# Kernel optimization log

Measured on AMD Instinct MI355X. Metric: run time of the kernel, lower is better.

Reference implementation:

```python
import jax, jax.numpy as jnp
import numpy as np

B, S, D, H, E = 1, 2048, 1024, 16, 65536
HD = D // H
LN_EPS = 1e-5


def setup_inputs() -> dict:
    key = jax.random.key(0)
    ks = jax.random.split(key, 18)
    s = 0.02
    inp = {
        'x': jax.random.normal(ks[0], (B, S, D), jnp.float32),
        'node_types': jax.random.uniform(ks[1], (B, S, 2), jnp.float32),
        'stoichiometry': jax.random.normal(ks[2], (E,), jnp.float32),
        'Wq': s * jax.random.normal(ks[3], (D, D), jnp.float32),
        'bq': jnp.zeros((D,), jnp.float32),
        'Wk': s * jax.random.normal(ks[4], (D, D), jnp.float32),
        'bk': jnp.zeros((D,), jnp.float32),
        'Wv': s * jax.random.normal(ks[5], (D, D), jnp.float32),
        'bv': jnp.zeros((D,), jnp.float32),
        'Wo': s * jax.random.normal(ks[6], (D, D), jnp.float32),
        'bo': jnp.zeros((D,), jnp.float32),
        'Wn1': s * jax.random.normal(ks[7], (D // 2, D + 2), jnp.float32),
        'bn1': jnp.zeros((D // 2,), jnp.float32),
        'Wn2': s * jax.random.normal(ks[8], (H, D // 2), jnp.float32),
        'bn2': jnp.zeros((H,), jnp.float32),
        'ln_g': jnp.ones((D,), jnp.float32),
        'ln_b': jnp.zeros((D,), jnp.float32),
        'edge_index': jax.random.randint(ks[9], (2, E), 0, S, jnp.int64),
    }
    return inp


def _layer_norm(y, g, b):
    m = jnp.mean(y, axis=-1, keepdims=True)
    v = jnp.mean(jnp.square(y - m), axis=-1, keepdims=True)
    return (y - m) * jax.lax.rsqrt(v + LN_EPS) * g + b


def reference(x, node_types, stoichiometry, Wq, bq, Wk, bk, Wv, bv, Wo, bo,
              Wn1, bn1, Wn2, bn2, ln_g, ln_b, edge_index):
    b, s, d = x.shape
    h, hd = H, d // H
    # QKV projections -> [b, h, s, hd]
    Q = (x @ Wq.T + bq).reshape(b, s, h, hd).transpose(0, 2, 1, 3)
    K = (x @ Wk.T + bk).reshape(b, s, h, hd).transpose(0, 2, 1, 3)
    V = (x @ Wv.T + bv).reshape(b, s, h, hd).transpose(0, 2, 1, 3)
    scores = jnp.einsum('bhqd,bhkd->bhqk', Q, K) / np.sqrt(hd)  # [b,h,s,s]
    # node-type attention MLP -> per-node, per-head weights [b,s,h]
    nt_in = jnp.concatenate([x, node_types], axis=-1)
    ntw = jax.nn.softmax(jax.nn.relu(nt_in @ Wn1.T + bn1) @ Wn2.T + bn2, axis=-1)
    # applied as per-head, per-key multiplicative mask [b,h,1,s]
    scores = scores * ntw.transpose(0, 2, 1)[:, :, None, :]
    # dense stoichiometric mask via edge scatter [s,s]
    stoich_mask = jnp.zeros((s, s), x.dtype).at[edge_index[0], edge_index[1]].set(stoichiometry)
    scores = scores * stoich_mask[None, None]
    attn = jax.nn.softmax(scores, axis=-1)  # dropout = identity (eval)
    out = jnp.einsum('bhqk,bhkd->bhqd', attn, V).transpose(0, 2, 1, 3).reshape(b, s, d)
    out = out @ Wo.T + bo
    y = _layer_norm(x + out, ln_g, ln_b)
    return (y, attn)
```

## Files before the change

### kernel.cpp

```cpp
#include <hip/hip_runtime.h>
#include <hip/hip_bf16.h>

#define S 2048
#define D 1024
#define NH 16
#define HD 64
#define NE 65536
#define DH 512
#define SLOTS 128

typedef __attribute__((ext_vector_type(8))) short short8;
typedef __attribute__((ext_vector_type(4))) float f32x4;

#define MFMA16(a, b, c) __builtin_amdgcn_mfma_f32_16x16x32_bf16(a, b, c, 0, 0, 0)

__device__ __forceinline__ unsigned short f2bf(float f) {
    __hip_bfloat16 h = __float2bfloat16(f);
    return *reinterpret_cast<unsigned short*>(&h);
}
__device__ __forceinline__ float bf2f(unsigned short u) {
    unsigned int x = ((unsigned int)u) << 16;
    return *reinterpret_cast<float*>(&x);
}

__device__ __forceinline__ void gload16(const unsigned short* g, unsigned short* l) {
    __builtin_amdgcn_global_load_lds(
        (const __attribute__((address_space(1))) unsigned int*)g,
        (__attribute__((address_space(3))) unsigned int*)l, 16, 0, 0);
}

__global__ __launch_bounds__(256) void k_prep(const float* __restrict__ x,
                                              const float* __restrict__ Wq,
                                              const float* __restrict__ Wk,
                                              const float* __restrict__ Wv,
                                              const float* __restrict__ Wn1,
                                              const float* __restrict__ Wo,
                                              const float* __restrict__ bq,
                                              const float* __restrict__ bk,
                                              const float* __restrict__ bv,
                                              const float* __restrict__ bn1,
                                              unsigned short* __restrict__ xb,
                                              unsigned short* __restrict__ wb,
                                              float* __restrict__ biasAll,
                                              int* __restrict__ rowcnt,
                                              float* __restrict__ vsumf) {
    int row = blockIdx.x, z = blockIdx.y, t = threadIdx.x;
    if (z == 5) {
        if (row < 14) {
            int g = row * 256 + t;
            float v = (g < 1024) ? bq[g]
                    : (g < 2048) ? bk[g - 1024]
                    : (g < 3072) ? bv[g - 2048] : bn1[g - 3072];
            biasAll[g] = v;
        } else if (row >= 16 && row < 24) {
            rowcnt[(row - 16) * 256 + t] = 0;
        } else if (row >= 24 && row < 28) {
            vsumf[(row - 24) * 256 + t] = 0.f;
        }
        return;
    }
    if (z >= 6) {
        int s = (z - 6) * 1024 + row;
        const float* r = x + (long)s * 1024;
        unsigned short* o = xb + (long)s * 1024;
#pragma unroll
        for (int j = 0; j < 4; j++) o[t * 4 + j] = f2bf(r[t * 4 + j]);
        return;
    }
    if (z == 3 && row >= DH) return;
    const float* src;
    long stride = 1024;
    if (z == 0) src = Wq;
    else if (z == 1) src = Wk;
    else if (z == 2) src = Wv;
    else if (z == 3) { src = Wn1; stride = 1026; }
    else src = Wo;
    const float* r = src + (long)row * stride;
    unsigned short* o = wb + (long)z * 1048576 + (long)row * 1024;
#pragma unroll
    for (int j = 0; j < 4; j++) o[t * 4 + j] = f2bf(r[t * 4 + j]);
}

__global__ __launch_bounds__(256) void k_gemm_fused(const unsigned short* __restrict__ A,
                                                    const unsigned short* __restrict__ Bw,
                                                    const float* __restrict__ biasAll,
                                                    const int* __restrict__ ei,
                                                    const float* __restrict__ st,
                                                    int* __restrict__ rowcnt,
                                                    int* __restrict__ cpack,
                                                    float* __restrict__ cval,
                                                    float* __restrict__ vsumf,
                                                    unsigned short* __restrict__ qout,
                                                    unsigned short* __restrict__ kout,
                                                    unsigned short* __restrict__ vout,
                                                    float* __restrict__ hidden) {
    if (blockIdx.y == 28) {
        int base = blockIdx.x * 4096 + threadIdx.x;
#pragma unroll
        for (int k = 0; k < 16; k++) {
            int e = base + k * 256;
            int r = ei[e], c = ei[NE + e];
            int i = atomicAdd(&rowcnt[r], 1);
            if (i < SLOTS) {
                cpack[r * SLOTS + i] = ((e + 1) << 11) | c;
                cval[r * SLOTS + i] = st[e];
            }
        }
        return;
    }
    __shared__ unsigned short Als[128 * 64];
    __shared__ unsigned short Bls[128 * 64];
    const int tid = threadIdx.x, w = tid >> 6, lane = tid & 63;
    const int l15 = lane & 15, lhi = lane >> 4;
    const int wr = w >> 1, wc = w & 1;
    const int m0 = blockIdx.x * 128, n0 = blockIdx.y * 128;
    f32x4 acc[4][4] = {};
    for (int kt = 0; kt < 16; kt++) {
        __syncthreads();
#pragma unroll
        for (int i = 0; i < 4; i++) {
            int reg = i * 4 + w;
            int idx = reg * 64 + lane;
            int row = idx >> 3, c8 = (idx & 7) * 8;
            gload16(A + (long)(m0 + row) * 1024 + kt * 64 + c8, Als + reg * 512);
            gload16(Bw + (long)(n0 + row) * 1024 + kt * 64 + c8, Bls + reg * 512);
        }
        asm volatile("s_waitcnt vmcnt(0)");
        __syncthreads();
#pragma unroll
        for (int kk = 0; kk < 2; kk++) {
            short8 a[4], b[4];
#pragma unroll
            for (int mi = 0; mi < 4; mi++)
                a[mi] = *reinterpret_cast<const short8*>(Als + (wr * 64 + mi * 16 + l15) * 64 + kk * 32 + lhi * 8);
#pragma unroll
            for (int ni = 0; ni < 4; ni++)
                b[ni] = *reinterpret_cast<const short8*>(Bls + (wc * 64 + ni * 16 + l15) * 64 + kk * 32 + lhi * 8);
#pragma unroll
            for (int mi = 0; mi < 4; mi++)
#pragma unroll
                for (int ni = 0; ni < 4; ni++)
                    acc[mi][ni] = MFMA16(a[mi], b[ni], acc[mi][ni]);
        }
    }
#pragma unroll
    for (int ni = 0; ni < 4; ni++) {
        int n = n0 + wc * 64 + ni * 16 + l15;
        float bb = biasAll[n];
        float colsum = 0.f;
#pragma unroll
        for (int mi = 0; mi < 4; mi++) {
#pragma unroll
            for (int r = 0; r < 4; r++) {
                int m = m0 + wr * 64 + mi * 16 + lhi * 4 + r;
                float v = acc[mi][ni][r] + bb;
                colsum += v;
                if (n < 3072) {
                    int z = n >> 10, c = n & 1023;
                    int hh = c >> 6, hd = c & 63;
                    unsigned short* dst = (z == 0) ? qout : ((z == 1) ? kout : vout);
                    dst[(long)hh * S * HD + (long)m * HD + hd] = f2bf(v);
                } else {
                    hidden[(long)m * DH + (n - 3072)] = v;
                }
            }
        }
        if (n >= 2048 && n < 3072) {
            colsum += __shfl_xor(colsum, 16);
            colsum += __shfl_xor(colsum, 32);
            if (lhi == 0) atomicAdd(&vsumf[n - 2048], colsum);
        }
    }
}

__global__ __launch_bounds__(256) void k_gemm_out(const unsigned short* __restrict__ A,
                                                  const unsigned short* __restrict__ Bw,
                                                  const float* __restrict__ bo,
                                                  float* __restrict__ proj) {
    __shared__ unsigned short Als[128 * 64];
    __shared__ unsigned short Bls[64 * 64];
    const int tid = threadIdx.x, w = tid >> 6, lane = tid & 63;
    const int l15 = lane & 15, lhi = lane >> 4;
    const int wr = w >> 1, wc = w & 1;
    const int m0 = blockIdx.x * 128, n0 = blockIdx.y * 64;
    f32x4 acc[4][2] = {};
    for (int kt = 0; kt < 16; kt++) {
        __syncthreads();
#pragma unroll
        for (int i = 0; i < 4; i++) {
            int reg = i * 4 + w;
            int idx = reg * 64 + lane;
            int row = idx >> 3, c8 = (idx & 7) * 8;
            gload16(A + (long)(m0 + row) * 1024 + kt * 64 + c8, Als + reg * 512);
        }
#pragma unroll
        for (int i = 0; i < 2; i++) {
            int reg = i * 4 + w;
            int idx = reg * 64 + lane;
            int row = idx >> 3, c8 = (idx & 7) * 8;
            gload16(Bw + (long)(n0 + row) * 1024 + kt * 64 + c8, Bls + reg * 512);
        }
        asm volatile("s_waitcnt vmcnt(0)");
        __syncthreads();
#pragma unroll
        for (int kk = 0; kk < 2; kk++) {
            short8 a[4], b[2];
#pragma unroll
            for (int mi = 0; mi < 4; mi++)
                a[mi] = *reinterpret_cast<const short8*>(Als + (wr * 64 + mi * 16 + l15) * 64 + kk * 32 + lhi * 8);
#pragma unroll
            for (int ni = 0; ni < 2; ni++)
                b[ni] = *reinterpret_cast<const short8*>(Bls + (wc * 32 + ni * 16 + l15) * 64 + kk * 32 + lhi * 8);
#pragma unroll
            for (int mi = 0; mi < 4; mi++)
#pragma unroll
                for (int ni = 0; ni < 2; ni++)
                    acc[mi][ni] = MFMA16(a[mi], b[ni], acc[mi][ni]);
        }
    }
#pragma unroll
    for (int ni = 0; ni < 2; ni++) {
        int n = n0 + wc * 32 + ni * 16 + l15;
        float bb = bo[n];
#pragma unroll
        for (int mi = 0; mi < 4; mi++) {
#pragma unroll
            for (int r = 0; r < 4; r++) {
                int m = m0 + wr * 64 + mi * 16 + lhi * 4 + r;
                proj[(long)m * 1024 + n] = acc[mi][ni][r] + bb;
            }
        }
    }
}

__global__ __launch_bounds__(256) void k_ntw(const float* __restrict__ hidden,
                                             const float* __restrict__ Wn1,
                                             const float* __restrict__ nt,
                                             const float* __restrict__ Wn2,
                                             const float* __restrict__ bn2,
                                             float* __restrict__ ntwT) {
    int tid = threadIdx.x;
    int s = blockIdx.x;
    __shared__ float rh[DH];
    __shared__ float part[16][17];
    float nt0 = nt[s * 2 + 0], nt1 = nt[s * 2 + 1];
    for (int j = tid; j < DH; j += 256) {
        float v = hidden[(long)s * DH + j] + nt0 * Wn1[(long)j * 1026 + 1024]
                + nt1 * Wn1[(long)j * 1026 + 1025];
        rh[j] = fmaxf(v, 0.f);
    }
    __syncthreads();
    {
        int hh = tid & 15, ch = tid >> 4;
        float p2 = 0.f;
#pragma unroll
        for (int j = 0; j < 32; j++) p2 += rh[ch * 32 + j] * Wn2[hh * DH + ch * 32 + j];
        part[ch][hh] = p2;
    }
    __syncthreads();
    if (tid < 16) {
        float l = bn2[tid];
#pragma unroll
        for (int c = 0; c < 16; c++) l += part[c][tid];
        float mx = l;
#pragma unroll
        for (int m = 1; m < 16; m <<= 1) mx = fmaxf(mx, __shfl_xor(mx, m));
        float e = __expf(l - mx);
        float sum = e;
#pragma unroll
        for (int m = 1; m < 16; m <<= 1) sum += __shfl_xor(sum, m);
        ntwT[tid * S + s] = e / sum;
    }
}

__global__ __launch_bounds__(256, 4) void k_sparsefill(const unsigned short* __restrict__ qb,
                                                       const unsigned short* __restrict__ kb,
                                                       const unsigned short* __restrict__ vb,
                                                       const float* __restrict__ ntwT,
                                                       const int* __restrict__ rowcnt,
                                                       const int* __restrict__ cpack,
                                                       const float* __restrict__ cval,
                                                       const float* __restrict__ vsumf,
                                                       float* __restrict__ attn_out,
                                                       unsigned short* __restrict__ pv_out) {
    __shared__ int c_lds[4][SLOTS];
    __shared__ float pd_lds[4][SLOTS];
    __shared__ unsigned char alive_lds[4][SLOTS];
    const int tid = threadIdx.x, w = tid >> 6, lane = tid & 63;
    int b = (int)blockIdx.x;
    b = (b & 7) * 1024 + (b >> 3);
    const int r = b * 4 + w;
    const int h = r >> 11, q = r & 2047;
    const int i_loc = lane & 15, dpart = lane >> 4;
    const int nnz_raw = rowcnt[q];
    const int nnz = nnz_raw < SLOTS ? nnz_raw : SLOTS;
    const int chunks = (nnz + 15) >> 4;

    for (int i = lane; i < nnz; i += 64) c_lds[w][i] = cpack[q * SLOTS + i];
    asm volatile("" ::: "memory");

    int myCnt = 0;
    for (int i = lane; i < nnz; i += 64) {
        int pk = c_lds[w][i];
        bool alive = true;
        for (int j = 0; j < nnz; j++) {
            int pj = c_lds[w][j];
            if ((((pj ^ pk) & 2047) == 0) && pj > pk) alive = false;
        }
        alive_lds[w][i] = alive ? 1 : 0;
        myCnt += alive ? 1 : 0;
    }
#pragma unroll
    for (int off = 1; off < 64; off <<= 1) myCnt += __shfl_xor(myCnt, off);
    const int nnz_alive = myCnt;
    asm volatile("" ::: "memory");

    float qf[16];
    {
        const unsigned short* qp = qb + ((long)h * S + q) * HD + dpart * 16;
        short8 q0 = *reinterpret_cast<const short8*>(qp);
        short8 q1 = *reinterpret_cast<const short8*>(qp + 8);
#pragma unroll
        for (int j = 0; j < 8; j++) {
            qf[j] = bf2f((unsigned short)q0[j]);
            qf[8 + j] = bf2f((unsigned short)q1[j]);
        }
    }

    float s_reg[8], e_reg[8];
    int c_reg[8];
    int vmask = 0;
#pragma unroll
    for (int c8 = 0; c8 < 8; c8++) {
        s_reg[c8] = -3.0e38f;
        c_reg[c8] = 0;
        if (c8 < chunks) {
            int i = c8 * 16 + i_loc;
            bool inr = i < nnz;
            int ig = inr ? i : 0;
            bool valid = inr && alive_lds[w][ig];
            int c = c_lds[w][ig] & 2047;
            float vv = cval[q * SLOTS + ig];
            const unsigned short* kp = kb + ((long)h * S + c) * HD + dpart * 16;
            short8 k0 = *reinterpret_cast<const short8*>(kp);
            short8 k1 = *reinterpret_cast<const short8*>(kp + 8);
            float dot = 0.f;
#pragma unroll
            for (int j = 0; j < 8; j++) {
                dot += qf[j] * bf2f((unsigned short)k0[j]);
                dot += qf[8 + j] * bf2f((unsigned short)k1[j]);
            }
            dot += __shfl_xor(dot, 16);
            dot += __shfl_xor(dot, 32);
            if (valid) {
                s_reg[c8] = dot * 0.125f * ntwT[(long)h * S + c] * vv;
                c_reg[c8] = c;
                vmask |= 1 << c8;
            }
        }
    }

    float m = s_reg[0];
#pragma unroll
    for (int c8 = 1; c8 < 8; c8++) m = fmaxf(m, s_reg[c8]);
    m = fmaxf(m, __shfl_xor(m, 1));
    m = fmaxf(m, __shfl_xor(m, 2));
    m = fmaxf(m, __shfl_xor(m, 4));
    m = fmaxf(m, __shfl_xor(m, 8));
    const float gm = fmaxf(m, 0.f);

    float zs = 0.f;
#pragma unroll
    for (int c8 = 0; c8 < 8; c8++) {
        e_reg[c8] = __expf(s_reg[c8] - gm);
        zs += e_reg[c8];
    }
    zs += __shfl_xor(zs, 1);
    zs += __shfl_xor(zs, 2);
    zs += __shfl_xor(zs, 4);
    zs += __shfl_xor(zs, 8);
    const float e0 = __expf(-gm);
    const float Z = zs + (float)(S - nnz_alive) * e0;
    const float inv = 1.0f / Z;
    const float p0 = e0 * inv;

    if (dpart == 0) {
#pragma unroll
        for (int c8 = 0; c8 < 8; c8++) {
            int i = c8 * 16 + i_loc;
            if (c8 < chunks && i < nnz)
                pd_lds[w][i] = ((vmask >> c8) & 1) ? e_reg[c8] * inv - p0 : 0.f;
        }
    }
    asm volatile("" ::: "memory");

    float* arow = attn_out + (long)r * S;
    f32x4* a4 = reinterpret_cast<f32x4*>(arow) + lane;
    const f32x4 f4 = {p0, p0, p0, p0};
#pragma unroll
    for (int u = 0; u < 8; u++) __builtin_nontemporal_store(f4, a4 + u * 64);
    __threadfence_block();
    if (dpart == 0) {
#pragma unroll
        for (int c8 = 0; c8 < 8; c8++)
            if ((vmask >> c8) & 1) arow[c_reg[c8]] = e_reg[c8] * inv;
    }

    float vacc = 0.f;
    for (int i = 0; i < nnz; i++) {
        int c = c_lds[w][i] & 2047;
        float pd = pd_lds[w][i];
        vacc += pd * bf2f(vb[((long)h * S + c) * HD + lane]);
    }
    vacc += p0 * vsumf[h * HD + lane];
    pv_out[(long)q * D + h * HD + lane] = f2bf(vacc);
}

__global__ __launch_bounds__(256) void k_ln(const float* __restrict__ x,
                                            const float* __restrict__ proj,
                                            const float* __restrict__ g,
                                            const float* __restrict__ bta,
                                            float* __restrict__ y) {
    int s = blockIdx.x, tid = threadIdx.x;
    int w = tid >> 6, lane = tid & 63;
    __shared__ float red[8];
    float4 xv = reinterpret_cast<const float4*>(x + (long)s * 1024)[tid];
    float4 pv = reinterpret_cast<const float4*>(proj + (long)s * 1024)[tid];
    float t0 = xv.x + pv.x, t1 = xv.y + pv.y, t2 = xv.z + pv.z, t3 = xv.w + pv.w;
    float lsum = t0 + t1 + t2 + t3;
#pragma unroll
    for (int m = 32; m >= 1; m >>= 1) lsum += __shfl_xor(lsum, m);
    if (lane == 0) red[w] = lsum;
    __syncthreads();
    float mean = (red[0] + red[1] + red[2] + red[3]) * (1.0f / 1024.f);
    float d0 = t0 - mean, d1 = t1 - mean, d2 = t2 - mean, d3 = t3 - mean;
    float lvar = d0 * d0 + d1 * d1 + d2 * d2 + d3 * d3;
#pragma unroll
    for (int m = 32; m >= 1; m >>= 1) lvar += __shfl_xor(lvar, m);
    if (lane == 0) red[4 + w] = lvar;
    __syncthreads();
    float var = (red[4] + red[5] + red[6] + red[7]) * (1.0f / 1024.f);
    float rstd = rsqrtf(var + 1e-5f);
    float4 gv = reinterpret_cast<const float4*>(g)[tid];
    float4 bv = reinterpret_cast<const float4*>(bta)[tid];
    float4 out;
    out.x = d0 * rstd * gv.x + bv.x;
    out.y = d1 * rstd * gv.y + bv.y;
    out.z = d2 * rstd * gv.z + bv.z;
    out.w = d3 * rstd * gv.w + bv.w;
    reinterpret_cast<float4*>(y + (long)s * 1024)[tid] = out;
}

extern "C" void kernel_launch(void* const* d_in, const int* in_sizes, int n_in,
                              void* d_out, int out_size, void* d_ws, size_t ws_size,
                              hipStream_t stream) {
    const float* x = (const float*)d_in[0];
    const float* node_types = (const float*)d_in[1];
    const float* stoich = (const float*)d_in[2];
    const float* Wq = (const float*)d_in[3];
    const float* bq = (const float*)d_in[4];
    const float* Wk = (const float*)d_in[5];
    const float* bk = (const float*)d_in[6];
    const float* Wv = (const float*)d_in[7];
    const float* bv = (const float*)d_in[8];
    const float* Wo = (const float*)d_in[9];
    const float* bo = (const float*)d_in[10];
    const float* Wn1 = (const float*)d_in[11];
    const float* bn1 = (const float*)d_in[12];
    const float* Wn2 = (const float*)d_in[13];
    const float* bn2 = (const float*)d_in[14];
    const float* ln_g = (const float*)d_in[15];
    const float* ln_b = (const float*)d_in[16];
    const int* ei = (const int*)d_in[17];

    char* ws = (char*)d_ws;
    unsigned short* x_bf = (unsigned short*)(ws);
    unsigned short* q_bf = (unsigned short*)(ws + (4l << 20));
    unsigned short* k_bf = (unsigned short*)(ws + (8l << 20));
    unsigned short* v_bf = (unsigned short*)(ws + (12l << 20));
    unsigned short* w_bf = (unsigned short*)(ws + (16l << 20));
    float* hidden = (float*)(ws + (26l << 20));
    float* ntwT = (float*)(ws + (30l << 20));
    int* rowcnt = (int*)(ws + (30l << 20) + (192l << 10));
    float* vsumf = (float*)(ws + (30l << 20) + (384l << 10));
    float* biasAll = (float*)(ws + (30l << 20) + (448l << 10));
    int* cpack = (int*)(ws + (31l << 20));
    float* cval = (float*)(ws + (32l << 20));
    unsigned short* pvb = (unsigned short*)(ws + (49l << 20));
    float* proj = (float*)(ws + (53l << 20));

    float* y_out = (float*)d_out;
    float* attn_out = (float*)d_out + (long)S * D;

    k_prep<<<dim3(1024, 8), 256, 0, stream>>>(x, Wq, Wk, Wv, Wn1, Wo,
                                              bq, bk, bv, bn1, x_bf, w_bf,
                                              biasAll, rowcnt, vsumf);
    k_gemm_fused<<<dim3(16, 29), 256, 0, stream>>>(x_bf, w_bf, biasAll,
                                                   ei, stoich, rowcnt, cpack, cval,
                                                   vsumf, q_bf, k_bf, v_bf, hidden);
    k_ntw<<<2048, 256, 0, stream>>>(hidden, Wn1, node_types, Wn2, bn2, ntwT);
    k_sparsefill<<<8192, 256, 0, stream>>>(q_bf, k_bf, v_bf, ntwT, rowcnt,
                                           cpack, cval, vsumf, attn_out, pvb);
    k_gemm_out<<<dim3(16, 16), 256, 0, stream>>>(pvb, w_bf + 4l * 1048576, bo, proj);
    k_ln<<<2048, 256, 0, stream>>>(x, proj, ln_g, ln_b, y_out);
}
```

Before: 154.9 us.

## Fuse all stages into one cooperative persistent kernel with grid syncs

Replaces the six separate kernel launches (prep, fused QKV GEMM plus edge bucketing, ntw MLP, sparse fill, output GEMM, layernorm) with a single cooperative kernel. Stages are separated by grid.sync and work items are distributed over a persistent grid of up to 512 blocks. The aim is to remove per-launch overhead and inter-kernel gaps. In exchange, occupancy is capped at two blocks per CU, blocks loop over work items, and every grid-wide barrier costs time and can expose load imbalance.

After: 498.9 us. 222% more time.

```diff
diff --git a/kernel.cpp b/kernel.cpp
--- a/kernel.cpp
+++ b/kernel.cpp
@@ -1,5 +1,8 @@
 #include <hip/hip_runtime.h>
+#include <hip/hip_cooperative_groups.h>
 #include <hip/hip_bf16.h>
+
+namespace cg = cooperative_groups;
 
 #define S 2048
 #define D 1024
@@ -29,478 +32,457 @@
         (__attribute__((address_space(3))) unsigned int*)l, 16, 0, 0);
 }
 
-__global__ __launch_bounds__(256) void k_prep(const float* __restrict__ x,
-                                              const float* __restrict__ Wq,
-                                              const float* __restrict__ Wk,
-                                              const float* __restrict__ Wv,
-                                              const float* __restrict__ Wn1,
-                                              const float* __restrict__ Wo,
-                                              const float* __restrict__ bq,
-                                              const float* __restrict__ bk,
-                                              const float* __restrict__ bv,
-                                              const float* __restrict__ bn1,
-                                              unsigned short* __restrict__ xb,
-                                              unsigned short* __restrict__ wb,
-                                              float* __restrict__ biasAll,
-                                              int* __restrict__ rowcnt,
-                                              float* __restrict__ vsumf) {
-    int row = blockIdx.x, z = blockIdx.y, t = threadIdx.x;
-    if (z == 5) {
-        if (row < 14) {
-            int g = row * 256 + t;
-            float v = (g < 1024) ? bq[g]
-                    : (g < 2048) ? bk[g - 1024]
-                    : (g < 3072) ? bv[g - 2048] : bn1[g - 3072];
-            biasAll[g] = v;
-        } else if (row >= 16 && row < 24) {
-            rowcnt[(row - 16) * 256 + t] = 0;
-        } else if (row >= 24 && row < 28) {
-            vsumf[(row - 24) * 256 + t] = 0.f;
-        }
-        return;
-    }
-    if (z >= 6) {
-        int s = (z - 6) * 1024 + row;
-        const float* r = x + (long)s * 1024;
-        unsigned short* o = xb + (long)s * 1024;
-#pragma unroll
-        for (int j = 0; j < 4; j++) o[t * 4 + j] = f2bf(r[t * 4 + j]);
-        return;
-    }
-    if (z == 3 && row >= DH) return;
-    const float* src;
-    long stride = 1024;
-    if (z == 0) src = Wq;
-    else if (z == 1) src = Wk;
-    else if (z == 2) src = Wv;
-    else if (z == 3) { src = Wn1; stride = 1026; }
-    else src = Wo;
-    const float* r = src + (long)row * stride;
-    unsigned short* o = wb + (long)z * 1048576 + (long)row * 1024;
-#pragma unroll
-    for (int j = 0; j < 4; j++) o[t * 4 + j] = f2bf(r[t * 4 + j]);
-}
-
-__global__ __launch_bounds__(256) void k_gemm_fused(const unsigned short* __restrict__ A,
-                                                    const unsigned short* __restrict__ Bw,
-                                                    const float* __restrict__ biasAll,
-                                                    const int* __restrict__ ei,
-                                                    const float* __restrict__ st,
-                                                    int* __restrict__ rowcnt,
-                                                    int* __restrict__ cpack,
-                                                    float* __restrict__ cval,
-                                                    float* __restrict__ vsumf,
-                                                    unsigned short* __restrict__ qout,
-                                                    unsigned short* __restrict__ kout,
-                                                    unsigned short* __restrict__ vout,
-                                                    float* __restrict__ hidden) {
-    if (blockIdx.y == 28) {
-        int base = blockIdx.x * 4096 + threadIdx.x;
-#pragma unroll
-        for (int k = 0; k < 16; k++) {
-            int e = base + k * 256;
-            int r = ei[e], c = ei[NE + e];
-            int i = atomicAdd(&rowcnt[r], 1);
-            if (i < SLOTS) {
-                cpack[r * SLOTS + i] = ((e + 1) << 11) | c;
-                cval[r * SLOTS + i] = st[e];
-            }
-        }
-        return;
-    }
-    __shared__ unsigned short Als[128 * 64];
-    __shared__ unsigned short Bls[128 * 64];
-    const int tid = threadIdx.x, w = tid >> 6, lane = tid & 63;
+struct Params {
+    const float *x, *nt, *st;
+    const float *Wq, *bq, *Wk, *bk, *Wv, *bv, *Wo, *bo;
+    const float *Wn1, *bn1, *Wn2, *bn2, *ln_g, *ln_b;
+    const int* ei;
+    unsigned short *xb, *wb, *qb, *kb, *vb, *pvb;
+    float *hidden, *ntwT, *vsumf, *biasAll, *cval, *proj, *attn, *y;
+    int *rowcnt, *cpack;
+};
+
+__global__ __launch_bounds__(256, 2) void k_mega(Params p) {
+    __shared__ __align__(16) unsigned char smem[32768];
+    cg::grid_group grid = cg::this_grid();
+    const int tid = threadIdx.x;
+    const int nb = gridDim.x, bid = blockIdx.x;
+    const int w = tid >> 6, lane = tid & 63;
     const int l15 = lane & 15, lhi = lane >> 4;
-    const int wr = w >> 1, wc = w & 1;
-    const int m0 = blockIdx.x * 128, n0 = blockIdx.y * 128;
-    f32x4 acc[4][4] = {};
-    for (int kt = 0; kt < 16; kt++) {
-        __syncthreads();
-#pragma unroll
-        for (int i = 0; i < 4; i++) {
-            int reg = i * 4 + w;
-            int idx = reg * 64 + lane;
-            int row = idx >> 3, c8 = (idx & 7) * 8;
-            gload16(A + (long)(m0 + row) * 1024 + kt * 64 + c8, Als + reg * 512);
-            gload16(Bw + (long)(n0 + row) * 1024 + kt * 64 + c8, Bls + reg * 512);
-        }
-        asm volatile("s_waitcnt vmcnt(0)");
-        __syncthreads();
-#pragma unroll
-        for (int kk = 0; kk < 2; kk++) {
-            short8 a[4], b[4];
-#pragma unroll
-            for (int mi = 0; mi < 4; mi++)
-                a[mi] = *reinterpret_cast<const short8*>(Als + (wr * 64 + mi * 16 + l15) * 64 + kk * 32 + lhi * 8);
-#pragma unroll
-            for (int ni = 0; ni < 4; ni++)
-                b[ni] = *reinterpret_cast<const short8*>(Bls + (wc * 64 + ni * 16 + l15) * 64 + kk * 32 + lhi * 8);
-#pragma unroll
-            for (int mi = 0; mi < 4; mi++)
-#pragma unroll
-                for (int ni = 0; ni < 4; ni++)
-                    acc[mi][ni] = MFMA16(a[mi], b[ni], acc[mi][ni]);
-        }
-    }
-#pragma unroll
-    for (int ni = 0; ni < 4; ni++) {
-        int n = n0 + wc * 64 + ni * 16 + l15;
-        float bb = biasAll[n];
-        float colsum = 0.f;
-#pragma unroll
-        for (int mi = 0; mi < 4; mi++) {
-#pragma unroll
-            for (int r = 0; r < 4; r++) {
-                int m = m0 + wr * 64 + mi * 16 + lhi * 4 + r;
-                float v = acc[mi][ni][r] + bb;
-                colsum += v;
-                if (n < 3072) {
-                    int z = n >> 10, c = n & 1023;
-                    int hh = c >> 6, hd = c & 63;
-                    unsigned short* dst = (z == 0) ? qout : ((z == 1) ? kout : vout);
-                    dst[(long)hh * S * HD + (long)m * HD + hd] = f2bf(v);
-                } else {
-                    hidden[(long)m * DH + (n - 3072)] = v;
-                }
-            }
-        }
-        if (n >= 2048 && n < 3072) {
-            colsum += __shfl_xor(colsum, 16);
-            colsum += __shfl_xor(colsum, 32);
-            if (lhi == 0) atomicAdd(&vsumf[n - 2048], colsum);
-        }
-    }
-}
-
-__global__ __launch_bounds__(256) void k_gemm_out(const unsigned short* __restrict__ A,
-                                                  const unsigned short* __restrict__ Bw,
-                                                  const float* __restrict__ bo,
-                                                  float* __restrict__ proj) {
-    __shared__ unsigned short Als[128 * 64];
-    __shared__ unsigned short Bls[64 * 64];
-    const int tid = threadIdx.x, w = tid >> 6, lane = tid & 63;
-    const int l15 = lane & 15, lhi = lane >> 4;
-    const int wr = w >> 1, wc = w & 1;
-    const int m0 = blockIdx.x * 128, n0 = blockIdx.y * 64;
-    f32x4 acc[4][2] = {};
-    for (int kt = 0; kt < 16; kt++) {
-        __syncthreads();
-#pragma unroll
-        for (int i = 0; i < 4; i++) {
-            int reg = i * 4 + w;
-            int idx = reg * 64 + lane;
-            int row = idx >> 3, c8 = (idx & 7) * 8;
-            gload16(A + (long)(m0 + row) * 1024 + kt * 64 + c8, Als + reg * 512);
-        }
-#pragma unroll
-        for (int i = 0; i < 2; i++) {
-            int reg = i * 4 + w;
-            int idx = reg * 64 + lane;
-            int row = idx >> 3, c8 = (idx & 7) * 8;
-            gload16(Bw + (long)(n0 + row) * 1024 + kt * 64 + c8, Bls + reg * 512);
-        }
-        asm volatile("s_waitcnt vmcnt(0)");
-        __syncthreads();
-#pragma unroll
-        for (int kk = 0; kk < 2; kk++) {
-            short8 a[4], b[2];
-#pragma unroll
-            for (int mi = 0; mi < 4; mi++)
-                a[mi] = *reinterpret_cast<const short8*>(Als + (wr * 64 + mi * 16 + l15) * 64 + kk * 32 + lhi * 8);
-#pragma unroll
-            for (int ni = 0; ni < 2; ni++)
-                b[ni] = *reinterpret_cast<const short8*>(Bls + (wc * 32 + ni * 16 + l15) * 64 + kk * 32 + lhi * 8);
-#pragma unroll
-            for (int mi = 0; mi < 4; mi++)
-#pragma unroll
-                for (int ni = 0; ni < 2; ni++)
-                    acc[mi][ni] = MFMA16(a[mi], b[ni], acc[mi][ni]);
-        }
-    }
-#pragma unroll
-    for (int ni = 0; ni < 2; ni++) {
-        int n = n0 + wc * 32 + ni * 16 + l15;
-        float bb = bo[n];
-#pragma unroll
-        for (int mi = 0; mi < 4; mi++) {
-#pragma unroll
-            for (int r = 0; r < 4; r++) {
-                int m = m0 + wr * 64 + mi * 16 + lhi * 4 + r;
-                proj[(long)m * 1024 + n] = acc[mi][ni][r] + bb;
-            }
-        }
-    }
-}
-
-__global__ __launch_bounds__(256) void k_ntw(const float* __restrict__ hidden,
-                                             const float* __restrict__ Wn1,
-                                             const float* __restrict__ nt,
-                                             const float* __restrict__ Wn2,
-                                             const float* __restrict__ bn2,
-                                             float* __restrict__ ntwT) {
-    int tid = threadIdx.x;
-    int s = blockIdx.x;
-    __shared__ float rh[DH];
-    __shared__ float part[16][17];
-    float nt0 = nt[s * 2 + 0], nt1 = nt[s * 2 + 1];
-    for (int j = tid; j < DH; j += 256) {
-        float v = hidden[(long)s * DH + j] + nt0 * Wn1[(long)j * 1026 + 1024]
-                + nt1 * Wn1[(long)j * 1026 + 1025];
-        rh[j] = fmaxf(v, 0.f);
-    }
-    __syncthreads();
+
+    for (int u = bid; u < 8192; u += nb) {
+        int row = u & 1023, z = u >> 10;
+        if (z == 5) {
+            if (row < 14) {
+                int g = row * 256 + tid;
+                float v = (g < 1024) ? p.bq[g]
+                        : (g < 2048) ? p.bk[g - 1024]
+                        : (g < 3072) ? p.bv[g - 2048] : p.bn1[g - 3072];
+                p.biasAll[g] = v;
+            } else if (row >= 16 && row < 24) {
+                p.rowcnt[(row - 16) * 256 + tid] = 0;
+            } else if (row >= 24 && row < 28) {
+                p.vsumf[(row - 24) * 256 + tid] = 0.f;
+            }
+            continue;
+        }
+        if (z >= 6) {
+            int s = (z - 6) * 1024 + row;
+            const float* r = p.x + (long)s * 1024;
+            unsigned short* o = p.xb + (long)s * 1024;
+#pragma unroll
+            for (int j = 0; j < 4; j++) o[tid * 4 + j] = f2bf(r[tid * 4 + j]);
+            continue;
+        }
+        if (z == 3 && row >= DH) continue;
+        const float* src;
+        long stride = 1024;
+        if (z == 0) src = p.Wq;
+        else if (z == 1) src = p.Wk;
+        else if (z == 2) src = p.Wv;
+        else if (z == 3) { src = p.Wn1; stride = 1026; }
+        else src = p.Wo;
+        const float* r = src + (long)row * stride;
+        unsigned short* o = p.wb + (long)z * 1048576 + (long)row * 1024;
+#pragma unroll
+        for (int j = 0; j < 4; j++) o[tid * 4 + j] = f2bf(r[tid * 4 + j]);
+    }
+    grid.sync();
+
     {
-        int hh = tid & 15, ch = tid >> 4;
-        float p2 = 0.f;
-#pragma unroll
-        for (int j = 0; j < 32; j++) p2 += rh[ch * 32 + j] * Wn2[hh * DH + ch * 32 + j];
-        part[ch][hh] = p2;
-    }
-    __syncthreads();
-    if (tid < 16) {
-        float l = bn2[tid];
-#pragma unroll
-        for (int c = 0; c < 16; c++) l += part[c][tid];
-        float mx = l;
-#pragma unroll
-        for (int m = 1; m < 16; m <<= 1) mx = fmaxf(mx, __shfl_xor(mx, m));
-        float e = __expf(l - mx);
-        float sum = e;
-#pragma unroll
-        for (int m = 1; m < 16; m <<= 1) sum += __shfl_xor(sum, m);
-        ntwT[tid * S + s] = e / sum;
-    }
-}
-
-__global__ __launch_bounds__(256, 4) void k_sparsefill(const unsigned short* __restrict__ qb,
-                                                       const unsigned short* __restrict__ kb,
-                                                       const unsigned short* __restrict__ vb,
-                                                       const float* __restrict__ ntwT,
-                                                       const int* __restrict__ rowcnt,
-                                                       const int* __restrict__ cpack,
-                                                       const float* __restrict__ cval,
-                                                       const float* __restrict__ vsumf,
-                                                       float* __restrict__ attn_out,
-                                                       unsigned short* __restrict__ pv_out) {
-    __shared__ int c_lds[4][SLOTS];
-    __shared__ float pd_lds[4][SLOTS];
-    __shared__ unsigned char alive_lds[4][SLOTS];
-    const int tid = threadIdx.x, w = tid >> 6, lane = tid & 63;
-    int b = (int)blockIdx.x;
-    b = (b & 7) * 1024 + (b >> 3);
-    const int r = b * 4 + w;
-    const int h = r >> 11, q = r & 2047;
-    const int i_loc = lane & 15, dpart = lane >> 4;
-    const int nnz_raw = rowcnt[q];
-    const int nnz = nnz_raw < SLOTS ? nnz_raw : SLOTS;
-    const int chunks = (nnz + 15) >> 4;
-
-    for (int i = lane; i < nnz; i += 64) c_lds[w][i] = cpack[q * SLOTS + i];
-    asm volatile("" ::: "memory");
-
-    int myCnt = 0;
-    for (int i = lane; i < nnz; i += 64) {
-        int pk = c_lds[w][i];
-        bool alive = true;
-        for (int j = 0; j < nnz; j++) {
-            int pj = c_lds[w][j];
-            if ((((pj ^ pk) & 2047) == 0) && pj > pk) alive = false;
-        }
-        alive_lds[w][i] = alive ? 1 : 0;
-        myCnt += alive ? 1 : 0;
-    }
-#pragma unroll
-    for (int off = 1; off < 64; off <<= 1) myCnt += __shfl_xor(myCnt, off);
-    const int nnz_alive = myCnt;
-    asm volatile("" ::: "memory");
-
-    float qf[16];
+        unsigned short* Als = (unsigned short*)smem;
+        unsigned short* Bls = (unsigned short*)(smem + 16384);
+        const int wr = w >> 1, wc = w & 1;
+        for (int u = bid; u < 464; u += nb) {
+            if (u >= 448) {
+                int base = (u - 448) * 4096 + tid;
+#pragma unroll
+                for (int k = 0; k < 16; k++) {
+                    int e = base + k * 256;
+                    int r = p.ei[e], c = p.ei[NE + e];
+                    int i = atomicAdd(&p.rowcnt[r], 1);
+                    if (i < SLOTS) {
+                        p.cpack[r * SLOTS + i] = ((e + 1) << 11) | c;
+                        p.cval[r * SLOTS + i] = p.st[e];
+                    }
+                }
+                continue;
+            }
+            const int m0 = (u & 15) * 128, n0 = (u >> 4) * 128;
+            f32x4 acc[4][4] = {};
+            for (int kt = 0; kt < 16; kt++) {
+                __syncthreads();
+#pragma unroll
+                for (int i = 0; i < 4; i++) {
+                    int reg = i * 4 + w;
+                    int idx = reg * 64 + lane;
+                    int row = idx >> 3, c8 = (idx & 7) * 8;
+                    gload16(p.xb + (long)(m0 + row) * 1024 + kt * 64 + c8, Als + reg * 512);
+                    gload16(p.wb + (long)(n0 + row) * 1024 + kt * 64 + c8, Bls + reg * 512);
+                }
+                asm volatile("s_waitcnt vmcnt(0)");
+                __syncthreads();
+#pragma unroll
+                for (int kk = 0; kk < 2; kk++) {
+                    short8 a[4], b[4];
+#pragma unroll
+                    for (int mi = 0; mi < 4; mi++)
+                        a[mi] = *reinterpret_cast<const short8*>(Als + (wr * 64 + mi * 16 + l15) * 64 + kk * 32 + lhi * 8);
+#pragma unroll
+                    for (int ni = 0; ni < 4; ni++)
+                        b[ni] = *reinterpret_cast<const short8*>(Bls + (wc * 64 + ni * 16 + l15) * 64 + kk * 32 + lhi * 8);
+#pragma unroll
+                    for (int mi = 0; mi < 4; mi++)
+#pragma unroll
+                        for (int ni = 0; ni < 4; ni++)
+                            acc[mi][ni] = MFMA16(a[mi], b[ni], acc[mi][ni]);
+                }
+            }
+#pragma unroll
+            for (int ni = 0; ni < 4; ni++) {
+                int n = n0 + wc * 64 + ni * 16 + l15;
+                float bb = p.biasAll[n];
+                float colsum = 0.f;
+#pragma unroll
+                for (int mi = 0; mi < 4; mi++) {
+#pragma unroll
+                    for (int r = 0; r < 4; r++) {
+                        int m = m0 + wr * 64 + mi * 16 + lhi * 4 + r;
+                        float v = acc[mi][ni][r] + bb;
+                        colsum += v;
+                        if (n < 3072) {
+                            int z = n >> 10, c = n & 1023;
+                            int hh = c >> 6, hd = c & 63;
+                            unsigned short* dst = (z == 0) ? p.qb : ((z == 1) ? p.kb : p.vb);
+                            dst[(long)hh * S * HD + (long)m * HD + hd] = f2bf(v);
+                        } else {
+                            p.hidden[(long)m * DH + (n - 3072)] = v;
+                        }
+                    }
+                }
+                if (n >= 2048 && n < 3072) {
+                    colsum += __shfl_xor(colsum, 16);
+                    colsum += __shfl_xor(colsum, 32);
+                    if (lhi == 0) atomicAdd(&p.vsumf[n - 2048], colsum);
+                }
+            }
+        }
+    }
+    grid.sync();
+
     {
-        const unsigned short* qp = qb + ((long)h * S + q) * HD + dpart * 16;
-        short8 q0 = *reinterpret_cast<const short8*>(qp);
-        short8 q1 = *reinterpret_cast<const short8*>(qp + 8);
-#pragma unroll
-        for (int j = 0; j < 8; j++) {
-            qf[j] = bf2f((unsigned short)q0[j]);
-            qf[8 + j] = bf2f((unsigned short)q1[j]);
-        }
-    }
-
-    float s_reg[8], e_reg[8];
-    int c_reg[8];
-    int vmask = 0;
-#pragma unroll
-    for (int c8 = 0; c8 < 8; c8++) {
-        s_reg[c8] = -3.0e38f;
-        c_reg[c8] = 0;
-        if (c8 < chunks) {
-            int i = c8 * 16 + i_loc;
-            bool inr = i < nnz;
-            int ig = inr ? i : 0;
-            bool valid = inr && alive_lds[w][ig];
-            int c = c_lds[w][ig] & 2047;
-            float vv = cval[q * SLOTS + ig];
-            const unsigned short* kp = kb + ((long)h * S + c) * HD + dpart * 16;
-            short8 k0 = *reinterpret_cast<const short8*>(kp);
-            short8 k1 = *reinterpret_cast<const short8*>(kp + 8);
-            float dot = 0.f;
-#pragma unroll
-            for (int j = 0; j < 8; j++) {
-                dot += qf[j] * bf2f((unsigned short)k0[j]);
-                dot += qf[8 + j] * bf2f((unsigned short)k1[j]);
-            }
-            dot += __shfl_xor(dot, 16);
-            dot += __shfl_xor(dot, 32);
-            if (valid) {
-                s_reg[c8] = dot * 0.125f * ntwT[(long)h * S + c] * vv;
-                c_reg[c8] = c;
-                vmask |= 1 << c8;
-            }
-        }
-    }
-
-    float m = s_reg[0];
-#pragma unroll
-    for (int c8 = 1; c8 < 8; c8++) m = fmaxf(m, s_reg[c8]);
-    m = fmaxf(m, __shfl_xor(m, 1));
-    m = fmaxf(m, __shfl_xor(m, 2));
-    m = fmaxf(m, __shfl_xor(m, 4));
-    m = fmaxf(m, __shfl_xor(m, 8));
-    const float gm = fmaxf(m, 0.f);
-
-    float zs = 0.f;
-#pragma unroll
-    for (int c8 = 0; c8 < 8; c8++) {
-        e_reg[c8] = __expf(s_reg[c8] - gm);
-        zs += e_reg[c8];
-    }
-    zs += __shfl_xor(zs, 1);
-    zs += __shfl_xor(zs, 2);
-    zs += __shfl_xor(zs, 4);
-    zs += __shfl_xor(zs, 8);
-    const float e0 = __expf(-gm);
-    const float Z = zs + (float)(S - nnz_alive) * e0;
-    const float inv = 1.0f / Z;
-    const float p0 = e0 * inv;
-
-    if (dpart == 0) {
-#pragma unroll
-        for (int c8 = 0; c8 < 8; c8++) {
-            int i = c8 * 16 + i_loc;
-            if (c8 < chunks && i < nnz)
-                pd_lds[w][i] = ((vmask >> c8) & 1) ? e_reg[c8] * inv - p0 : 0.f;
-        }
-    }
-    asm volatile("" ::: "memory");
-
-    float* arow = attn_out + (long)r * S;
-    f32x4* a4 = reinterpret_cast<f32x4*>(arow) + lane;
-    const f32x4 f4 = {p0, p0, p0, p0};
-#pragma unroll
-    for (int u = 0; u < 8; u++) __builtin_nontemporal_store(f4, a4 + u * 64);
-    __threadfence_block();
-    if (dpart == 0) {
-#pragma unroll
-        for (int c8 = 0; c8 < 8; c8++)
-            if ((vmask >> c8) & 1) arow[c_reg[c8]] = e_reg[c8] * inv;
-    }
-
-    float vacc = 0.f;
-    for (int i = 0; i < nnz; i++) {
-        int c = c_lds[w][i] & 2047;
-        float pd = pd_lds[w][i];
-        vacc += pd * bf2f(vb[((long)h * S + c) * HD + lane]);
-    }
-    vacc += p0 * vsumf[h * HD + lane];
-    pv_out[(long)q * D + h * HD + lane] = f2bf(vacc);
-}
-
-__global__ __launch_bounds__(256) void k_ln(const float* __restrict__ x,
-                                            const float* __restrict__ proj,
-                                            const float* __restrict__ g,
-                                            const float* __restrict__ bta,
-                                            float* __restrict__ y) {
-    int s = blockIdx.x, tid = threadIdx.x;
-    int w = tid >> 6, lane = tid & 63;
-    __shared__ float red[8];
-    float4 xv = reinterpret_cast<const float4*>(x + (long)s * 1024)[tid];
-    float4 pv = reinterpret_cast<const float4*>(proj + (long)s * 1024)[tid];
-    float t0 = xv.x + pv.x, t1 = xv.y + pv.y, t2 = xv.z + pv.z, t3 = xv.w + pv.w;
-    float lsum = t0 + t1 + t2 + t3;
-#pragma unroll
-    for (int m = 32; m >= 1; m >>= 1) lsum += __shfl_xor(lsum, m);
-    if (lane == 0) red[w] = lsum;
-    __syncthreads();
-    float mean = (red[0] + red[1] + red[2] + red[3]) * (1.0f / 1024.f);
-    float d0 = t0 - mean, d1 = t1 - mean, d2 = t2 - mean, d3 = t3 - mean;
-    float lvar = d0 * d0 + d1 * d1 + d2 * d2 + d3 * d3;
-#pragma unroll
-    for (int m = 32; m >= 1; m >>= 1) lvar += __shfl_xor(lvar, m);
-    if (lane == 0) red[4 + w] = lvar;
-    __syncthreads();
-    float var = (red[4] + red[5] + red[6] + red[7]) * (1.0f / 1024.f);
-    float rstd = rsqrtf(var + 1e-5f);
-    float4 gv = reinterpret_cast<const float4*>(g)[tid];
-    float4 bv = reinterpret_cast<const float4*>(bta)[tid];
-    float4 out;
-    out.x = d0 * rstd * gv.x + bv.x;
-    out.y = d1 * rstd * gv.y + bv.y;
-    out.z = d2 * rstd * gv.z + bv.z;
-    out.w = d3 * rstd * gv.w + bv.w;
-    reinterpret_cast<float4*>(y + (long)s * 1024)[tid] = out;
+        float* rh = (float*)smem;
+        float (*part)[17] = (float(*)[17])(smem + 2048);
+        for (int s = bid; s < 2048; s += nb) {
+            float nt0 = p.nt[s * 2 + 0], nt1 = p.nt[s * 2 + 1];
+            for (int j = tid; j < DH; j += 256) {
+                float v = p.hidden[(long)s * DH + j] + nt0 * p.Wn1[(long)j * 1026 + 1024]
+                        + nt1 * p.Wn1[(long)j * 1026 + 1025];
+                rh[j] = fmaxf(v, 0.f);
+            }
+            __syncthreads();
+            {
+                int hh = tid & 15, ch = tid >> 4;
+                float p2 = 0.f;
+#pragma unroll
+                for (int j = 0; j < 32; j++) p2 += rh[ch * 32 + j] * p.Wn2[hh * DH + ch * 32 + j];
+                part[ch][hh] = p2;
+            }
+            __syncthreads();
+            if (tid < 16) {
+                float l = p.bn2[tid];
+#pragma unroll
+                for (int c = 0; c < 16; c++) l += part[c][tid];
+                float mx = l;
+#pragma unroll
+                for (int m = 1; m < 16; m <<= 1) mx = fmaxf(mx, __shfl_xor(mx, m));
+                float e = __expf(l - mx);
+                float sum = e;
+#pragma unroll
+                for (int m = 1; m < 16; m <<= 1) sum += __shfl_xor(sum, m);
+                p.ntwT[tid * S + s] = e / sum;
+            }
+            __syncthreads();
+        }
+    }
+    grid.sync();
+
+    {
+        int (*c_lds)[SLOTS] = (int(*)[SLOTS])smem;
+        float (*pd_lds)[SLOTS] = (float(*)[SLOTS])(smem + 2048);
+        unsigned char (*alive_lds)[SLOTS] = (unsigned char(*)[SLOTS])(smem + 4096);
+        const int i_loc = lane & 15, dpart = lane >> 4;
+        for (int u = bid; u < 8192; u += nb) {
+            int up = (u & 7) * 1024 + (u >> 3);
+            const int r = up * 4 + w;
+            const int h = r >> 11, q = r & 2047;
+            const int nnz_raw = p.rowcnt[q];
+            const int nnz = nnz_raw < SLOTS ? nnz_raw : SLOTS;
+            const int chunks = (nnz + 15) >> 4;
+
+            for (int i = lane; i < nnz; i += 64) c_lds[w][i] = p.cpack[q * SLOTS + i];
+            asm volatile("" ::: "memory");
+
+            int myCnt = 0;
+            for (int i = lane; i < nnz; i += 64) {
+                int pk = c_lds[w][i];
+                bool alive = true;
+                for (int j = 0; j < nnz; j++) {
+                    int pj = c_lds[w][j];
+                    if ((((pj ^ pk) & 2047) == 0) && pj > pk) alive = false;
+                }
+                alive_lds[w][i] = alive ? 1 : 0;
+                myCnt += alive ? 1 : 0;
+            }
+#pragma unroll
+            for (int off = 1; off < 64; off <<= 1) myCnt += __shfl_xor(myCnt, off);
+            const int nnz_alive = myCnt;
+            asm volatile("" ::: "memory");
+
+            float qf[16];
+            {
+                const unsigned short* qp = p.qb + ((long)h * S + q) * HD + dpart * 16;
+                short8 q0 = *reinterpret_cast<const short8*>(qp);
+                short8 q1 = *reinterpret_cast<const short8*>(qp + 8);
+#pragma unroll
+                for (int j = 0; j < 8; j++) {
+                    qf[j] = bf2f((unsigned short)q0[j]);
+                    qf[8 + j] = bf2f((unsigned short)q1[j]);
+                }
+            }
+
+            float s_reg[8], e_reg[8];
+            int c_reg[8];
+            int vmask = 0;
+#pragma unroll
+            for (int c8 = 0; c8 < 8; c8++) {
+                s_reg[c8] = -3.0e38f;
+                c_reg[c8] = 0;
+                if (c8 < chunks) {
+                    int i = c8 * 16 + i_loc;
+                    bool inr = i < nnz;
+                    int ig = inr ? i : 0;
+                    bool valid = inr && alive_lds[w][ig];
+                    int c = c_lds[w][ig] & 2047;
+                    float vv = p.cval[q * SLOTS + ig];
+                    const unsigned short* kp = p.kb + ((long)h * S + c) * HD + dpart * 16;
+                    short8 k0 = *reinterpret_cast<const short8*>(kp);
+                    short8 k1 = *reinterpret_cast<const short8*>(kp + 8);
+                    float dot = 0.f;
+#pragma unroll
+                    for (int j = 0; j < 8; j++) {
+                        dot += qf[j] * bf2f((unsigned short)k0[j]);
+                        dot += qf[8 + j] * bf2f((unsigned short)k1[j]);
+                    }
+                    dot += __shfl_xor(dot, 16);
+                    dot += __shfl_xor(dot, 32);
+                    if (valid) {
+                        s_reg[c8] = dot * 0.125f * p.ntwT[(long)h * S + c] * vv;
+                        c_reg[c8] = c;
+                        vmask |= 1 << c8;
+                    }
+                }
+            }
+
+            float m = s_reg[0];
+#pragma unroll
+            for (int c8 = 1; c8 < 8; c8++) m = fmaxf(m, s_reg[c8]);
+            m = fmaxf(m, __shfl_xor(m, 1));
+            m = fmaxf(m, __shfl_xor(m, 2));
+            m = fmaxf(m, __shfl_xor(m, 4));
+            m = fmaxf(m, __shfl_xor(m, 8));
+            const float gm = fmaxf(m, 0.f);
+
+            float zs = 0.f;
+#pragma unroll
+            for (int c8 = 0; c8 < 8; c8++) {
+                e_reg[c8] = __expf(s_reg[c8] - gm);
+                zs += e_reg[c8];
+            }
+            zs += __shfl_xor(zs, 1);
+            zs += __shfl_xor(zs, 2);
+            zs += __shfl_xor(zs, 4);
+            zs += __shfl_xor(zs, 8);
+            const float e0 = __expf(-gm);
+            const float Z = zs + (float)(S - nnz_alive) * e0;
+            const float inv = 1.0f / Z;
+            const float p0 = e0 * inv;
+
+            if (dpart == 0) {
+#pragma unroll
+                for (int c8 = 0; c8 < 8; c8++) {
+                    int i = c8 * 16 + i_loc;
+                    if (c8 < chunks && i < nnz)
+                        pd_lds[w][i] = ((vmask >> c8) & 1) ? e_reg[c8] * inv - p0 : 0.f;
+                }
+            }
+            asm volatile("" ::: "memory");
+
+            float* arow = p.attn + (long)r * S;
+            f32x4* a4 = reinterpret_cast<f32x4*>(arow) + lane;
+            const f32x4 f4 = {p0, p0, p0, p0};
+#pragma unroll
+            for (int uu = 0; uu < 8; uu++) __builtin_nontemporal_store(f4, a4 + uu * 64);
+            __threadfence_block();
+            if (dpart == 0) {
+#pragma unroll
+                for (int c8 = 0; c8 < 8; c8++)
+                    if ((vmask >> c8) & 1) arow[c_reg[c8]] = e_reg[c8] * inv;
+            }
+
+            float vacc = 0.f;
+            for (int i = 0; i < nnz; i++) {
+                int c = c_lds[w][i] & 2047;
+                float pd = pd_lds[w][i];
+                vacc += pd * bf2f(p.vb[((long)h * S + c) * HD + lane]);
+            }
+            vacc += p0 * p.vsumf[h * HD + lane];
+            p.pvb[(long)q * D + h * HD + lane] = f2bf(vacc);
+        }
+    }
+    grid.sync();
+
+    {
+        unsigned short* Als = (unsigned short*)smem;
+        unsigned short* Bls = (unsigned short*)(smem + 16384);
+        const int wr = w >> 1, wc = w & 1;
+        for (int u = bid; u < 256; u += nb) {
+            const int m0 = (u & 15) * 128, n0 = (u >> 4) * 64;
+            f32x4 acc[4][2] = {};
+            for (int kt = 0; kt < 16; kt++) {
+                __syncthreads();
+#pragma unroll
+                for (int i = 0; i < 4; i++) {
+                    int reg = i * 4 + w;
+                    int idx = reg * 64 + lane;
+                    int row = idx >> 3, c8 = (idx & 7) * 8;
+                    gload16(p.pvb + (long)(m0 + row) * 1024 + kt * 64 + c8, Als + reg * 512);
+                }
+#pragma unroll
+                for (int i = 0; i < 2; i++) {
+                    int reg = i * 4 + w;
+                    int idx = reg * 64 + lane;
+                    int row = idx >> 3, c8 = (idx & 7) * 8;
+                    gload16(p.wb + 4l * 1048576 + (long)(n0 + row) * 1024 + kt * 64 + c8, Bls + reg * 512);
+                }
+                asm volatile("s_waitcnt vmcnt(0)");
+                __syncthreads();
+#pragma unroll
+                for (int kk = 0; kk < 2; kk++) {
+                    short8 a[4], b[2];
+#pragma unroll
+                    for (int mi = 0; mi < 4; mi++)
+                        a[mi] = *reinterpret_cast<const short8*>(Als + (wr * 64 + mi * 16 + l15) * 64 + kk * 32 + lhi * 8);
+#pragma unroll
+                    for (int ni = 0; ni < 2; ni++)
+                        b[ni] = *reinterpret_cast<const short8*>(Bls + (wc * 32 + ni * 16 + l15) * 64 + kk * 32 + lhi * 8);
+#pragma unroll
+                    for (int mi = 0; mi < 4; mi++)
+#pragma unroll
+                        for (int ni = 0; ni < 2; ni++)
+                            acc[mi][ni] = MFMA16(a[mi], b[ni], acc[mi][ni]);
+                }
+            }
+#pragma unroll
+            for (int ni = 0; ni < 2; ni++) {
+                int n = n0 + wc * 32 + ni * 16 + l15;
+                float bb = p.bo[n];
+#pragma unroll
+                for (int mi = 0; mi < 4; mi++) {
+#pragma unroll
+                    for (int r = 0; r < 4; r++) {
+                        int m = m0 + wr * 64 + mi * 16 + lhi * 4 + r;
+                        p.proj[(long)m * 1024 + n] = acc[mi][ni][r] + bb;
+                    }
+                }
+            }
+        }
+    }
+    grid.sync();
+
+    {
+        float* red = (float*)smem;
+        for (int s = bid; s < 2048; s += nb) {
+            float4 xv = reinterpret_cast<const float4*>(p.x + (long)s * 1024)[tid];
+            float4 pv = reinterpret_cast<const float4*>(p.proj + (long)s * 1024)[tid];
+            float t0 = xv.x + pv.x, t1 = xv.y + pv.y, t2 = xv.z + pv.z, t3 = xv.w + pv.w;
+            float lsum = t0 + t1 + t2 + t3;
+#pragma unroll
+            for (int m = 32; m >= 1; m >>= 1) lsum += __shfl_xor(lsum, m);
+            if (lane == 0) red[w] = lsum;
+            __syncthreads();
+            float mean = (red[0] + red[1] + red[2] + red[3]) * (1.0f / 1024.f);
+            float d0 = t0 - mean, d1 = t1 - mean, d2 = t2 - mean, d3 = t3 - mean;
+            float lvar = d0 * d0 + d1 * d1 + d2 * d2 + d3 * d3;
+#pragma unroll
+            for (int m = 32; m >= 1; m >>= 1) lvar += __shfl_xor(lvar, m);
+            if (lane == 0) red[4 + w] = lvar;
+            __syncthreads();
+            float var = (red[4] + red[5] + red[6] + red[7]) * (1.0f / 1024.f);
+            float rstd = rsqrtf(var + 1e-5f);
+            float4 gv = reinterpret_cast<const float4*>(p.ln_g)[tid];
+            float4 bv = reinterpret_cast<const float4*>(p.ln_b)[tid];
+            float4 out;
+            out.x = d0 * rstd * gv.x + bv.x;
+            out.y = d1 * rstd * gv.y + bv.y;
+            out.z = d2 * rstd * gv.z + bv.z;
+            out.w = d3 * rstd * gv.w + bv.w;
+            reinterpret_cast<float4*>(p.y + (long)s * 1024)[tid] = out;
+            __syncthreads();
+        }
+    }
 }
 
 extern "C" void kernel_launch(void* const* d_in, const int* in_sizes, int n_in,
                               void* d_out, int out_size, void* d_ws, size_t ws_size,
                               hipStream_t stream) {
-    const float* x = (const float*)d_in[0];
-    const float* node_types = (const float*)d_in[1];
-    const float* stoich = (const float*)d_in[2];
-    const float* Wq = (const float*)d_in[3];
-    const float* bq = (const float*)d_in[4];
-    const float* Wk = (const float*)d_in[5];
-    const float* bk = (const float*)d_in[6];
-    const float* Wv = (const float*)d_in[7];
-    const float* bv = (const float*)d_in[8];
-    const float* Wo = (const float*)d_in[9];
-    const float* bo = (const float*)d_in[10];
-    const float* Wn1 = (const float*)d_in[11];
-    const float* bn1 = (const float*)d_in[12];
-    const float* Wn2 = (const float*)d_in[13];
-    const float* bn2 = (const float*)d_in[14];
-    const float* ln_g = (const float*)d_in[15];
-    const float* ln_b = (const float*)d_in[16];
-    const int* ei = (const int*)d_in[17];
-
     char* ws = (char*)d_ws;
-    unsigned short* x_bf = (unsigned short*)(ws);
-    unsigned short* q_bf = (unsigned short*)(ws + (4l << 20));
-    unsigned short* k_bf = (unsigned short*)(ws + (8l << 20));
-    unsigned short* v_bf = (unsigned short*)(ws + (12l << 20));
-    unsigned short* w_bf = (unsigned short*)(ws + (16l << 20));
-    float* hidden = (float*)(ws + (26l << 20));
-    float* ntwT = (float*)(ws + (30l << 20));
-    int* rowcnt = (int*)(ws + (30l << 20) + (192l << 10));
-    float* vsumf = (float*)(ws + (30l << 20) + (384l << 10));
-    float* biasAll = (float*)(ws + (30l << 20) + (448l << 10));
-    int* cpack = (int*)(ws + (31l << 20));
-    float* cval = (float*)(ws + (32l << 20));
-    unsigned short* pvb = (unsigned short*)(ws + (49l << 20));
-    float* proj = (float*)(ws + (53l << 20));
-
-    float* y_out = (float*)d_out;
-    float* attn_out = (float*)d_out + (long)S * D;
-
-    k_prep<<<dim3(1024, 8), 256, 0, stream>>>(x, Wq, Wk, Wv, Wn1, Wo,
-                                              bq, bk, bv, bn1, x_bf, w_bf,
-                                              biasAll, rowcnt, vsumf);
-    k_gemm_fused<<<dim3(16, 29), 256, 0, stream>>>(x_bf, w_bf, biasAll,
-                                                   ei, stoich, rowcnt, cpack, cval,
-                                                   vsumf, q_bf, k_bf, v_bf, hidden);
-    k_ntw<<<2048, 256, 0, stream>>>(hidden, Wn1, node_types, Wn2, bn2, ntwT);
-    k_sparsefill<<<8192, 256, 0, stream>>>(q_bf, k_bf, v_bf, ntwT, rowcnt,
-                                           cpack, cval, vsumf, attn_out, pvb);
-    k_gemm_out<<<dim3(16, 16), 256, 0, stream>>>(pvb, w_bf + 4l * 1048576, bo, proj);
-    k_ln<<<2048, 256, 0, stream>>>(x, proj, ln_g, ln_b, y_out);
+    Params p;
+    p.x = (const float*)d_in[0];
+    p.nt = (const float*)d_in[1];
+    p.st = (const float*)d_in[2];
+    p.Wq = (const float*)d_in[3];
+    p.bq = (const float*)d_in[4];
+    p.Wk = (const float*)d_in[5];
+    p.bk = (const float*)d_in[6];
+    p.Wv = (const float*)d_in[7];
+    p.bv = (const float*)d_in[8];
+    p.Wo = (const float*)d_in[9];
+    p.bo = (const float*)d_in[10];
+    p.Wn1 = (const float*)d_in[11];
+    p.bn1 = (const float*)d_in[12];
+    p.Wn2 = (const float*)d_in[13];
+    p.bn2 = (const float*)d_in[14];
+    p.ln_g = (const float*)d_in[15];
+    p.ln_b = (const float*)d_in[16];
+    p.ei = (const int*)d_in[17];
+
+    p.xb = (unsigned short*)(ws);
+    p.qb = (unsigned short*)(ws + (4l << 20));
+    p.kb = (unsigned short*)(ws + (8l << 20));
+    p.vb = (unsigned short*)(ws + (12l << 20));
+    p.wb = (unsigned short*)(ws + (16l << 20));
+    p.hidden = (float*)(ws + (26l << 20));
+    p.ntwT = (float*)(ws + (30l << 20));
+    p.rowcnt = (int*)(ws + (30l << 20) + (192l << 10));
+    p.vsumf = (float*)(ws + (30l << 20) + (384l << 10));
+    p.biasAll = (float*)(ws + (30l << 20) + (448l << 10));
+    p.cpack = (int*)(ws + (31l << 20));
+    p.cval = (float*)(ws + (32l << 20));
+    p.pvb = (unsigned short*)(ws + (49l << 20));
+    p.proj = (float*)(ws + (53l << 20));
+
+    p.y = (float*)d_out;
+    p.attn = (float*)d_out + (long)S * D;
+
+    int maxBlocksPerCU = 2;
+    (void)hipOccupancyMaxActiveBlocksPerMultiprocessor(&maxBlocksPerCU,
+                                                       (const void*)k_mega, 256, 0);
+    if (maxBlocksPerCU < 1) maxBlocksPerCU = 1;
+    int grid = maxBlocksPerCU * 256;
+    if (grid > 512) grid = 512;
+
+    void* args[] = {&p};
+    hipLaunchCooperativeKernel((const void*)k_mega, dim3(grid), dim3(256),
+                               args, 0, stream);
 }
```
